# Performance work log

Hardware: AMD Instinct MI355X
Metric: run time of the kernel (lower is better)

The kernel has to match this reference:

```python
import jax, jax.numpy as jnp
import numpy as np

T = 36
N_POLES = 40
LAM = 0.1
MAX_ITER = 100
TOL = 1e-4
B, P = 2, 4096


def build_dictionary(Drr, Dtheta):
    # rows i = 0..T-1; columns: [rr^i cos(i th), (-rr)^i cos(i th), rr^i sin(i th), (-rr)^i sin(i th)]
    i = jnp.arange(T, dtype=Drr.dtype)[:, None]              # [T,1]
    pr = jnp.power(Drr[None, :], i)                          # rr^i   [T,N]
    sign = jnp.power(jnp.asarray(-1.0, Drr.dtype), i)        # (-1)^i [T,1]
    c = jnp.cos(i * Dtheta[None, :])
    s = jnp.sin(i * Dtheta[None, :])
    dic = jnp.concatenate([pr * c, sign * pr * c, pr * s, sign * pr * s], axis=1)  # [T,4N]
    G = jnp.linalg.norm(dic, axis=0)                         # column norms
    G = jnp.where(G == 0, jnp.sqrt(jnp.asarray(float(T), dic.dtype)), G)
    return dic / G


def soft_shrink(v, lambd):
    return jnp.sign(v) * jnp.maximum(jnp.abs(v) - lambd, 0.0)


def fista(D, Y, lam, max_iter=MAX_ITER):
    DtD = D.T @ D                                            # [4N,4N]
    L = jnp.linalg.norm(DtD)                                 # torch.norm(DtD, 2) = Frobenius norm
    linv = 1.0 / L
    DtY = jnp.einsum('tk,btp->bkp', D, Y) * linv             # [B,4N,P]
    K = DtD.shape[0]
    A = jnp.eye(K, dtype=D.dtype) - DtD * linv               # [4N,4N]
    lambd = lam * linv
    Bb, _, Pp = DtY.shape

    # FISTA momentum coefficients are data independent -> precompute
    ts = np.ones(max_iter + 1)
    for k in range(max_iter):
        ts[k + 1] = (1 + np.sqrt(1 + 4 * ts[k] ** 2)) / 2.0
    tts = jnp.asarray((ts[:-1] - 1) / ts[1:], dtype=D.dtype)  # [max_iter]

    x0 = jnp.zeros((Bb, K, Pp), dtype=D.dtype)

    def step(carry, inputs):
        x_old, y_old, done = carry
        tt, k = inputs
        x_new = soft_shrink(jnp.einsum('kj,bjp->bkp', A, y_old) + DtY, lambd)
        y_new = x_new * (1 + tt) - x_old * tt
        # torch divides by x_old.shape[1]: P on the first check (x_old is the 2-D zeros init), 4N after
        denom = jnp.where(k == 0, float(Pp), float(K)).astype(x_new.dtype)
        conv = jnp.linalg.norm(x_old - x_new) / denom < TOL
        x_out = jnp.where(done, x_old, x_new)
        y_out = jnp.where(done, y_old, y_new)
        return (x_out, y_out, jnp.logical_or(done, conv)), None

    (x_fin, _, _), _ = jax.lax.scan(step, (x0, x0, jnp.array(False)),
                                    (tts, jnp.arange(max_iter)))
    return x_fin


def setup_inputs() -> dict:
    key = jax.random.key(0)
    k1, k2, k3 = jax.random.split(key, 3)
    Drr = jax.random.uniform(k1, (N_POLES,), dtype=jnp.float32)
    Dtheta = jax.random.uniform(k2, (N_POLES,), dtype=jnp.float32)
    x = jax.random.normal(k3, (B, T, P), dtype=jnp.float32)
    return {"Drr": Drr, "Dtheta": Dtheta, "x": x}


def reference(Drr, Dtheta, x):
    dic = build_dictionary(Drr, Dtheta)   # [T, 4N]
    sparsecode = fista(dic, x, LAM)       # [B, 4N, P]
    return sparsecode
```

## Files before the change

### kernel.cpp

```cpp
#include <hip/hip_runtime.h>
#include <hip/hip_bf16.h>

#define TT 36
#define KK 160
#define NPOLE 40
#define PP 4096
#define MAXIT 100
#define COLS 16
#define NG 2
#define NWC 4
#define NTHR 512
#define YS 168
#define GRID 256

#define WS_LINV  0
#define WS_LAMBD 1
#define WS_TTS   2
#define WS_FROB  132
#define WS_D     512
#define WS_A     6400
#define WS_AH    32000
#define WS_AL    44800

typedef float  floatx4 __attribute__((ext_vector_type(4)));
typedef short  shortx8 __attribute__((ext_vector_type(8)));

__device__ __forceinline__ short f2bf(float v) {
  unsigned u = __float_as_uint(v);
  unsigned r = (u + 0x7FFFu + ((u >> 16) & 1u)) >> 16;
  return (short)r;
}
__device__ __forceinline__ float bf2f(short s) {
  return __uint_as_float(((unsigned)(unsigned short)s) << 16);
}

__global__ void setup1(const float* __restrict__ Drr,
                       const float* __restrict__ Dth,
                       float* __restrict__ ws) {
  __shared__ float Dl[TT * KK];
  __shared__ float Gl[KK];
  const int tid = threadIdx.x;
  if (tid == 0) ws[WS_FROB] = 0.f;

  for (int idx = tid; idx < TT * KK; idx += 256) {
    int i = idx / KK, k = idx % KK;
    int g = k / NPOLE, n = k % NPOLE;
    float rr = Drr[n], th = Dth[n];
    float pr = powf(rr, (float)i);
    float ang = (float)i * th;
    float tri = (g < 2) ? cosf(ang) : sinf(ang);
    float sgn = ((g & 1) && (i & 1)) ? -1.0f : 1.0f;
    Dl[idx] = pr * tri * sgn;
  }
  __syncthreads();
  if (tid < KK) {
    float s = 0.f;
    for (int i = 0; i < TT; i++) { float v = Dl[i * KK + tid]; s += v * v; }
    float gn = sqrtf(s);
    Gl[tid] = (gn == 0.f) ? sqrtf((float)TT) : gn;
  }
  __syncthreads();
  for (int idx = tid; idx < TT * KK; idx += 256)
    ws[WS_D + idx] = Dl[idx] / Gl[idx % KK];

  if (tid == 0) {
    double ts = 1.0;
    for (int k = 0; k < MAXIT; k++) {
      double tn = (1.0 + sqrt(1.0 + 4.0 * ts * ts)) * 0.5;
      ws[WS_TTS + k] = (float)((ts - 1.0) / tn);
      ts = tn;
    }
  }
}

__global__ void setup2(float* __restrict__ ws) {
  __shared__ float red[256];
  const int a = blockIdx.x, b = threadIdx.x;
  const float* D = &ws[WS_D];
  float ss = 0.f;
  if (b < KK) {
    float s = 0.f;
    for (int t = 0; t < TT; t++) s += D[t * KK + a] * D[t * KK + b];
    ws[WS_A + a * KK + b] = s;
    ss = s * s;
  }
  red[b] = ss;
  __syncthreads();
  for (int off = 128; off > 0; off >>= 1) {
    if (b < off) red[b] += red[b + off];
    __syncthreads();
  }
  if (b == 0) atomicAdd(&ws[WS_FROB], red[0]);
}

__global__ void setup3(float* __restrict__ ws) {
  const int idx = blockIdx.x * 256 + threadIdx.x;
  const float linv = 1.0f / sqrtf(ws[WS_FROB]);
  short* AHs = (short*)&ws[WS_AH];
  short* ALs = (short*)&ws[WS_AL];
  if (idx < KK * KK) {
    int a = idx / KK, b = idx % KK;
    float av = ((a == b) ? 1.0f : 0.0f) - ws[WS_A + idx] * linv;
    short h = f2bf(av);
    AHs[idx] = h;
    ALs[idx] = f2bf(av - bf2f(h));
  }
  if (idx == 0) { ws[WS_LINV] = linv; ws[WS_LAMBD] = 0.1f * linv; }
}

__global__ __launch_bounds__(NTHR, 2)
void fista_kernel(const float* __restrict__ x, float* __restrict__ out,
                  float* __restrict__ ws) {
  __shared__ __align__(16) short ys[NG][2][COLS * YS];
  __shared__ float ttsl[MAXIT];
  __shared__ unsigned cnt[NG];

  const int tid  = threadIdx.x;
  const int w    = tid >> 6;
  const int lane = tid & 63;
  const int quad = lane >> 4;
  const int l16  = lane & 15;
  const int g    = w >> 2;
  const int v    = w & 3;
  const int bid  = blockIdx.x;
  const int bb   = (bid * 32) / PP;
  const int p0   = (bid * 32) % PP + 16 * g;
  const float linv  = ws[WS_LINV];
  const float lambd = ws[WS_LAMBD];
  const float adiag = 1.0f - linv;

  int base, nrs;
  if (g == 0) { base = (v < 2) ? 48 * v : 32 * v + 32; nrs = (v < 2) ? 3 : 2; }
  else        { base = (v < 2) ? 32 * v : 48 * v - 32; nrs = (v < 2) ? 2 : 3; }

  for (int i = tid; i < MAXIT; i += NTHR) ttsl[i] = ws[WS_TTS + i];

  const short* AH = (const short*)&ws[WS_AH];
  const short* AL = (const short*)&ws[WS_AL];
  shortx8 ah[3][5], al[3][5];
#pragma unroll
  for (int rs = 0; rs < 3; rs++) {
    if (rs < nrs) {
#pragma unroll
      for (int kc = 0; kc < 5; kc++) {
        int off = (base + 16 * rs + l16) * KK + 32 * kc + 8 * quad;
        ah[rs][kc] = *(const shortx8*)&AH[off];
        al[rs][kc] = *(const shortx8*)&AL[off];
      }
    }
  }

  const float* Dg = &ws[WS_D];
  float dty[3][4] = {{0.f,0.f,0.f,0.f},{0.f,0.f,0.f,0.f},{0.f,0.f,0.f,0.f}};
  {
    const float* xcol = &x[(size_t)bb * TT * PP + p0 + l16];
    for (int t = 0; t < TT; t++) {
      float xv = xcol[(size_t)t * PP];
#pragma unroll
      for (int rs = 0; rs < 3; rs++) {
        if (rs < nrs) {
          float4 d = *(const float4*)&Dg[t * KK + base + 16 * rs + 4 * quad];
          dty[rs][0] = fmaf(d.x, xv, dty[rs][0]);
          dty[rs][1] = fmaf(d.y, xv, dty[rs][1]);
          dty[rs][2] = fmaf(d.z, xv, dty[rs][2]);
          dty[rs][3] = fmaf(d.w, xv, dty[rs][3]);
        }
      }
    }
#pragma unroll
    for (int rs = 0; rs < 3; rs++)
#pragma unroll
      for (int r = 0; r < 4; r++) dty[rs][r] *= linv;
  }

  {
    int* z = (int*)&ys[0][0][0];
    for (int i = tid; i < NG * 2 * COLS * YS / 2; i += NTHR) z[i] = 0;
    if (tid < NG) cnt[tid] = 0;
  }
  float xo[3][4] = {{0.f,0.f,0.f,0.f},{0.f,0.f,0.f,0.f},{0.f,0.f,0.f,0.f}};
  float yl[3][4] = {{0.f,0.f,0.f,0.f},{0.f,0.f,0.f,0.f},{0.f,0.f,0.f,0.f}};
  __syncthreads();

  if (g == 1) __builtin_amdgcn_s_sleep(10);

  for (int it = 0; it < MAXIT; it++) {
    if (it > 0) {
      const unsigned tgt = (unsigned)(NWC * it);
      while (__atomic_load_n(&cnt[g], __ATOMIC_ACQUIRE) < tgt)
        __builtin_amdgcn_s_sleep(1);
    }
    const short* yb = &ys[g][it & 1][0];
    const int cb = l16 * YS + 8 * quad;
    floatx4 accM[3] = {{dty[0][0], dty[0][1], dty[0][2], dty[0][3]},
                       {dty[1][0], dty[1][1], dty[1][2], dty[1][3]},
                       {dty[2][0], dty[2][1], dty[2][2], dty[2][3]}};
    floatx4 accB[3] = {{0.f,0.f,0.f,0.f},{0.f,0.f,0.f,0.f},{0.f,0.f,0.f,0.f}};
#pragma unroll
    for (int kc = 0; kc < 5; kc++) {
      shortx8 bh = *(const shortx8*)&yb[cb + 32 * kc];
#pragma unroll
      for (int rs = 0; rs < 3; rs++) {
        if (rs < nrs) {
          accM[rs] = __builtin_amdgcn_mfma_f32_16x16x32_bf16(ah[rs][kc], bh, accM[rs], 0, 0, 0);
          accB[rs] = __builtin_amdgcn_mfma_f32_16x16x32_bf16(al[rs][kc], bh, accB[rs], 0, 0, 0);
        }
      }
    }

    const float tt = ttsl[it];
    short* yw = &ys[g][(it & 1) ^ 1][0];
#pragma unroll
    for (int rs = 0; rs < 3; rs++) {
      if (rs < nrs) {
        float yn[4];
#pragma unroll
        for (int r = 0; r < 4; r++) {
          float vv = fmaf(adiag, yl[rs][r], accM[rs][r] + accB[rs][r]);
          float cl = __builtin_amdgcn_fmed3f(vv, -lambd, lambd);
          float xv = vv - cl;
          yn[r] = fmaf(tt, xv - xo[rs][r], xv);
          xo[rs][r] = xv;
        }
        __hip_bfloat162 h01 = __float22bfloat162_rn(make_float2(yn[0], yn[1]));
        __hip_bfloat162 h23 = __float22bfloat162_rn(make_float2(yn[2], yn[3]));
        unsigned u01 = *(unsigned*)&h01;
        unsigned u23 = *(unsigned*)&h23;
        yl[rs][0] = yn[0] - __uint_as_float(u01 << 16);
        yl[rs][1] = yn[1] - __uint_as_float(u01 & 0xffff0000u);
        yl[rs][2] = yn[2] - __uint_as_float(u23 << 16);
        yl[rs][3] = yn[3] - __uint_as_float(u23 & 0xffff0000u);
        const int ko = l16 * YS + base + 16 * rs + 4 * quad;
        *(uint2*)&yw[ko] = make_uint2(u01, u23);
      }
    }

    if (lane == 0) __atomic_fetch_add(&cnt[g], 1u, __ATOMIC_RELEASE);
  }

#pragma unroll
  for (int rs = 0; rs < 3; rs++) {
    if (rs < nrs) {
#pragma unroll
      for (int r = 0; r < 4; r++)
        out[((size_t)bb * KK + base + 16 * rs + 4 * quad + r) * PP + p0 + l16] = xo[rs][r];
    }
  }
}

extern "C" void kernel_launch(void* const* d_in, const int* in_sizes, int n_in,
                              void* d_out, int out_size, void* d_ws, size_t ws_size,
                              hipStream_t stream) {
  const float* Drr = (const float*)d_in[0];
  const float* Dth = (const float*)d_in[1];
  const float* x   = (const float*)d_in[2];
  float* out = (float*)d_out;
  float* ws  = (float*)d_ws;

  setup1<<<1, 256, 0, stream>>>(Drr, Dth, ws);
  setup2<<<160, 256, 0, stream>>>(ws);
  setup3<<<100, 256, 0, stream>>>(ws);
  fista_kernel<<<GRID, NTHR, 0, stream>>>(x, out, ws);
}
```

Baseline: 189.5 us.

## Use single fp16 MFMA for A matrix, start on own chunk before waiting

Replaces the bf16 hi/lo split of A (two MFMAs per tile) with a single fp16 copy of A, halving MFMA work and A register usage. The diagonal rounding error is corrected in fp32 using the full y value, and y is exchanged as fp16 with an fp32 residual. Each wave first issues the MFMA for the K-chunk it wrote itself before spinning on the group counter, overlapping the wait with compute, and wave priority is raised around compute. Lower precision in the off-diagonal A entries risks numerical drift relative to the fp32 reference.

```diff
diff --git a/kernel.cpp b/kernel.cpp
--- a/kernel.cpp
+++ b/kernel.cpp
@@ -1,5 +1,6 @@
 #include <hip/hip_runtime.h>
 #include <hip/hip_bf16.h>
+#include <hip/hip_fp16.h>
 
 #define TT 36
 #define KK 160
@@ -22,17 +23,9 @@
 #define WS_AH    32000
 #define WS_AL    44800
 
-typedef float  floatx4 __attribute__((ext_vector_type(4)));
-typedef short  shortx8 __attribute__((ext_vector_type(8)));
-
-__device__ __forceinline__ short f2bf(float v) {
-  unsigned u = __float_as_uint(v);
-  unsigned r = (u + 0x7FFFu + ((u >> 16) & 1u)) >> 16;
-  return (short)r;
-}
-__device__ __forceinline__ float bf2f(short s) {
-  return __uint_as_float(((unsigned)(unsigned short)s) << 16);
-}
+typedef float    floatx4 __attribute__((ext_vector_type(4)));
+typedef short    shortx8 __attribute__((ext_vector_type(8)));
+typedef _Float16 halfx8  __attribute__((ext_vector_type(8)));
 
 __global__ void setup1(const float* __restrict__ Drr,
                        const float* __restrict__ Dth,
@@ -96,14 +89,11 @@
 __global__ void setup3(float* __restrict__ ws) {
   const int idx = blockIdx.x * 256 + threadIdx.x;
   const float linv = 1.0f / sqrtf(ws[WS_FROB]);
-  short* AHs = (short*)&ws[WS_AH];
-  short* ALs = (short*)&ws[WS_AL];
+  _Float16* AHs = (_Float16*)&ws[WS_AH];
   if (idx < KK * KK) {
     int a = idx / KK, b = idx % KK;
-    float av = ((a == b) ? 1.0f : 0.0f) - ws[WS_A + idx] * linv;
-    short h = f2bf(av);
-    AHs[idx] = h;
-    ALs[idx] = f2bf(av - bf2f(h));
+    float av = (a == b) ? (1.0f - linv) : (0.0f - ws[WS_A + idx] * linv);
+    AHs[idx] = (_Float16)av;
   }
   if (idx == 0) { ws[WS_LINV] = linv; ws[WS_LAMBD] = 0.1f * linv; }
 }
@@ -128,6 +118,8 @@
   const float linv  = ws[WS_LINV];
   const float lambd = ws[WS_LAMBD];
   const float adiag = 1.0f - linv;
+  const float ahf   = (float)(_Float16)adiag;
+  const float ddiag = adiag - ahf;
 
   int base, nrs;
   if (g == 0) { base = (v < 2) ? 48 * v : 32 * v + 32; nrs = (v < 2) ? 3 : 2; }
@@ -135,17 +127,15 @@
 
   for (int i = tid; i < MAXIT; i += NTHR) ttsl[i] = ws[WS_TTS + i];
 
-  const short* AH = (const short*)&ws[WS_AH];
-  const short* AL = (const short*)&ws[WS_AL];
-  shortx8 ah[3][5], al[3][5];
+  const _Float16* AH = (const _Float16*)&ws[WS_AH];
+  halfx8 ah[3][5];
 #pragma unroll
   for (int rs = 0; rs < 3; rs++) {
     if (rs < nrs) {
 #pragma unroll
       for (int kc = 0; kc < 5; kc++) {
         int off = (base + 16 * rs + l16) * KK + 32 * kc + 8 * quad;
-        ah[rs][kc] = *(const shortx8*)&AH[off];
-        al[rs][kc] = *(const shortx8*)&AL[off];
+        ah[rs][kc] = *(const halfx8*)&AH[off];
       }
     }
   }
@@ -180,32 +170,49 @@
   }
   float xo[3][4] = {{0.f,0.f,0.f,0.f},{0.f,0.f,0.f,0.f},{0.f,0.f,0.f,0.f}};
   float yl[3][4] = {{0.f,0.f,0.f,0.f},{0.f,0.f,0.f,0.f},{0.f,0.f,0.f,0.f}};
+  float yv[3][4] = {{0.f,0.f,0.f,0.f},{0.f,0.f,0.f,0.f},{0.f,0.f,0.f,0.f}};
   __syncthreads();
 
   if (g == 1) __builtin_amdgcn_s_sleep(10);
+  __builtin_amdgcn_s_setprio(1);
+
+#define RD_MFMA(KC) { \
+    halfx8 bh = *(const halfx8*)&yb[cb + 32 * (KC)]; \
+    _Pragma("unroll") \
+    for (int rs = 0; rs < 3; rs++) \
+      if (rs < nrs) \
+        accM[rs] = __builtin_amdgcn_mfma_f32_16x16x32_f16(ah[rs][KC], bh, accM[rs], 0, 0, 0); \
+  }
+
+#define ITER_BODY(SK, K1, K2, K3, K4) { \
+    RD_MFMA(SK) \
+    if (it > 0) { \
+      const unsigned tgt = (unsigned)(NWC * it); \
+      __builtin_amdgcn_s_setprio(0); \
+      while (__atomic_load_n(&cnt[g], __ATOMIC_ACQUIRE) < tgt) \
+        __builtin_amdgcn_s_sleep(1); \
+      __builtin_amdgcn_s_setprio(1); \
+    } \
+    RD_MFMA(K1) RD_MFMA(K2) RD_MFMA(K3) RD_MFMA(K4) \
+  }
 
   for (int it = 0; it < MAXIT; it++) {
-    if (it > 0) {
-      const unsigned tgt = (unsigned)(NWC * it);
-      while (__atomic_load_n(&cnt[g], __ATOMIC_ACQUIRE) < tgt)
-        __builtin_amdgcn_s_sleep(1);
-    }
     const short* yb = &ys[g][it & 1][0];
     const int cb = l16 * YS + 8 * quad;
     floatx4 accM[3] = {{dty[0][0], dty[0][1], dty[0][2], dty[0][3]},
                        {dty[1][0], dty[1][1], dty[1][2], dty[1][3]},
                        {dty[2][0], dty[2][1], dty[2][2], dty[2][3]}};
-    floatx4 accB[3] = {{0.f,0.f,0.f,0.f},{0.f,0.f,0.f,0.f},{0.f,0.f,0.f,0.f}};
-#pragma unroll
-    for (int kc = 0; kc < 5; kc++) {
-      shortx8 bh = *(const shortx8*)&yb[cb + 32 * kc];
-#pragma unroll
-      for (int rs = 0; rs < 3; rs++) {
-        if (rs < nrs) {
-          accM[rs] = __builtin_amdgcn_mfma_f32_16x16x32_bf16(ah[rs][kc], bh, accM[rs], 0, 0, 0);
-          accB[rs] = __builtin_amdgcn_mfma_f32_16x16x32_bf16(al[rs][kc], bh, accB[rs], 0, 0, 0);
-        }
-      }
+
+    if (g == 0) {
+      if      (v == 0) ITER_BODY(0, 1, 2, 3, 4)
+      else if (v == 1) ITER_BODY(2, 0, 1, 3, 4)
+      else if (v == 2) ITER_BODY(3, 0, 1, 2, 4)
+      else             ITER_BODY(4, 0, 1, 2, 3)
+    } else {
+      if      (v == 0) ITER_BODY(0, 1, 2, 3, 4)
+      else if (v == 1) ITER_BODY(1, 0, 2, 3, 4)
+      else if (v == 2) ITER_BODY(2, 0, 1, 3, 4)
+      else             ITER_BODY(4, 0, 1, 2, 3)
     }
 
     const float tt = ttsl[it];
@@ -216,20 +223,22 @@
         float yn[4];
 #pragma unroll
         for (int r = 0; r < 4; r++) {
-          float vv = fmaf(adiag, yl[rs][r], accM[rs][r] + accB[rs][r]);
+          float vv = fmaf(ddiag, yv[rs][r], fmaf(ahf, yl[rs][r], accM[rs][r]));
           float cl = __builtin_amdgcn_fmed3f(vv, -lambd, lambd);
           float xv = vv - cl;
           yn[r] = fmaf(tt, xv - xo[rs][r], xv);
           xo[rs][r] = xv;
         }
-        __hip_bfloat162 h01 = __float22bfloat162_rn(make_float2(yn[0], yn[1]));
-        __hip_bfloat162 h23 = __float22bfloat162_rn(make_float2(yn[2], yn[3]));
-        unsigned u01 = *(unsigned*)&h01;
-        unsigned u23 = *(unsigned*)&h23;
-        yl[rs][0] = yn[0] - __uint_as_float(u01 << 16);
-        yl[rs][1] = yn[1] - __uint_as_float(u01 & 0xffff0000u);
-        yl[rs][2] = yn[2] - __uint_as_float(u23 << 16);
-        yl[rs][3] = yn[3] - __uint_as_float(u23 & 0xffff0000u);
+        _Float16 h0 = (_Float16)yn[0], h1 = (_Float16)yn[1];
+        _Float16 h2 = (_Float16)yn[2], h3 = (_Float16)yn[3];
+        yl[rs][0] = yn[0] - (float)h0;  yv[rs][0] = yn[0];
+        yl[rs][1] = yn[1] - (float)h1;  yv[rs][1] = yn[1];
+        yl[rs][2] = yn[2] - (float)h2;  yv[rs][2] = yn[2];
+        yl[rs][3] = yn[3] - (float)h3;  yv[rs][3] = yn[3];
+        unsigned u01 = (unsigned)__builtin_bit_cast(unsigned short, h0) |
+                       ((unsigned)__builtin_bit_cast(unsigned short, h1) << 16);
+        unsigned u23 = (unsigned)__builtin_bit_cast(unsigned short, h2) |
+                       ((unsigned)__builtin_bit_cast(unsigned short, h3) << 16);
         const int ko = l16 * YS + base + 16 * rs + 4 * quad;
         *(uint2*)&yw[ko] = make_uint2(u01, u23);
       }
```

Result: faster. 183.8 us (-3.0%).
